# Kernel tuning notes

Hardware: AMD Instinct MI355X
Metric: run time of the kernel (lower is better)

## Reference

```python
import jax, jax.numpy as jnp
import numpy as np

USER = 50000
ITEM = 50000
N = USER + ITEM
LATDIM = 64
N_EDGES = 3200000
GNN_LAYERS = 2
RIS_ADJ_LAMBDA = 0.2
RIS_LAMBDA = 0.5
LEAK = 0.2


def l2norm(x, eps=1e-12):
    # F.normalize(x, dim=1)
    n = jnp.sqrt(jnp.sum(x * x, axis=1, keepdims=True))
    return x / jnp.maximum(n, eps)


def spmm(rows, cols, vals, x):
    # sparse [N,N] @ dense [N,D] via gather + segment-sum
    return jax.ops.segment_sum(vals[:, None] * x[cols], rows, num_segments=N)


def gcn_layer(rows, cols, vals, embeds, att_w):
    e = spmm(rows, cols, vals, embeds)                     # [N, D]
    scores = e @ att_w                                     # [N]
    att = jax.nn.softmax(scores, axis=0)[:, None]          # softmax over nodes
    return jax.nn.leaky_relu(e * att, negative_slope=LEAK) # dropout = identity (eval)


def setup_inputs() -> dict:
    key = jax.random.key(0)
    ks = jax.random.split(key, 16)
    d = {}
    for i, pre in enumerate(["adj", "img", "txt"]):
        d[pre + "_rows"] = jax.random.randint(ks[3 * i], (N_EDGES,), 0, N, dtype=jnp.int32)
        d[pre + "_cols"] = jax.random.randint(ks[3 * i + 1], (N_EDGES,), 0, N, dtype=jnp.int32)
        d[pre + "_vals"] = jax.random.uniform(ks[3 * i + 2], (N_EDGES,), dtype=jnp.float32)
    d["u_embeds"] = jax.random.normal(ks[9], (USER, LATDIM), dtype=jnp.float32) * 0.1
    d["i_embeds"] = jax.random.normal(ks[10], (ITEM, LATDIM), dtype=jnp.float32) * 0.1
    d["img_W"] = jax.random.normal(ks[11], (1024, LATDIM), dtype=jnp.float32) * 0.03
    d["img_b"] = jnp.zeros((LATDIM,), dtype=jnp.float32)
    d["txt_W"] = jax.random.normal(ks[12], (384, LATDIM), dtype=jnp.float32) * 0.05
    d["txt_b"] = jnp.zeros((LATDIM,), dtype=jnp.float32)
    d["modal_weight"] = jnp.array([0.5, 0.5], dtype=jnp.float32)
    d["att_w"] = jax.random.normal(ks[13], (GNN_LAYERS, LATDIM), dtype=jnp.float32) * 0.1
    d["image_embedding"] = jax.random.normal(ks[14], (USER, 1024), dtype=jnp.float32)
    d["text_embedding"] = jax.random.normal(ks[15], (USER, 384), dtype=jnp.float32)
    return d


def reference(adj_rows, adj_cols, adj_vals,
              img_rows, img_cols, img_vals,
              txt_rows, txt_cols, txt_vals,
              u_embeds, i_embeds,
              img_W, img_b, txt_W, txt_b,
              modal_weight, att_w,
              image_embedding, text_embedding):
    # modality projection (args.trans == 1: Linear layers)
    image_feats = image_embedding @ img_W + img_b          # [item, D]
    text_feats = text_embedding @ txt_W + txt_b            # [item, D]
    weight = jax.nn.softmax(modal_weight)

    e0 = jnp.concatenate([u_embeds, i_embeds])             # [N, D]

    embeds_image_adj = spmm(img_rows, img_cols, img_vals, e0)
    embeds_image = jnp.concatenate([u_embeds, l2norm(image_feats)])
    embeds_image_ = jnp.concatenate([embeds_image[:USER], i_embeds])
    embeds_image_ = spmm(adj_rows, adj_cols, adj_vals, embeds_image_)
    embeds_image = embeds_image + embeds_image_

    embeds_text_adj = spmm(txt_rows, txt_cols, txt_vals, e0)
    embeds_text = jnp.concatenate([u_embeds, l2norm(text_feats)])
    embeds_text = spmm(adj_rows, adj_cols, adj_vals, embeds_text)
    embeds_text_ = jnp.concatenate([embeds_text[:USER], i_embeds])
    embeds_text_ = spmm(adj_rows, adj_cols, adj_vals, embeds_text_)
    embeds_text = embeds_text + embeds_text_

    embeds_image = embeds_image + RIS_ADJ_LAMBDA * embeds_image_adj
    embeds_text = embeds_text + RIS_ADJ_LAMBDA * embeds_text_adj
    embeds_modal = weight[0] * embeds_image + weight[1] * embeds_text

    embeds = embeds_modal
    total = embeds_modal
    for l in range(GNN_LAYERS):
        embeds = gcn_layer(adj_rows, adj_cols, adj_vals, embeds, att_w[l])
        total = total + embeds
    out = total + RIS_LAMBDA * l2norm(embeds_modal)
    return out[:USER], out[USER:]
```

## Files before the change

kernel.cpp:

```cpp
#include <hip/hip_runtime.h>
#include <hip/hip_bf16.h>

#define LEAK 0.2f

__device__ __forceinline__ float wave_sum(float p) {
#pragma unroll
  for (int m = 1; m < 64; m <<= 1) p += __shfl_xor(p, m);
  return p;
}

__device__ __forceinline__ int wave_scan_incl(int v) {
  int lane = threadIdx.x & 63;
#pragma unroll
  for (int d = 1; d < 64; d <<= 1) {
    int t = __shfl_up(v, d);
    if (lane >= d) v += t;
  }
  return v;
}

__global__ __launch_bounds__(256) void gemm_bias(
    const float* __restrict__ A, const float* __restrict__ W,
    const float* __restrict__ bias, float* __restrict__ out, int M, int K)
{
  __shared__ float As[64 * 132];
  __shared__ float Wt[64 * 132];
  const int tid = threadIdx.x;
  const int lane = tid & 63, wave = tid >> 6;
  const int c0 = lane & 15;
  const int rsub = lane >> 4;
  const int rloc = wave * 16 + rsub * 4;
  const int rowBase = blockIdx.x * 64;

  float acc[4][4];
#pragma unroll
  for (int r = 0; r < 4; ++r)
#pragma unroll
    for (int i = 0; i < 4; ++i) acc[r][i] = 0.f;

  for (int kc = 0; kc < K; kc += 128) {
    __syncthreads();
#pragma unroll
    for (int j = 0; j < 8; ++j) {
      int idx = tid + j * 256;
      int row = idx >> 5, k4 = idx & 31;
      int gr = rowBase + row;
      int gk = kc + k4 * 4;
      float4 av = make_float4(0.f, 0.f, 0.f, 0.f);
      if (gr < M && gk < K) av = *(const float4*)(A + (size_t)gr * K + gk);
      *(float4*)(As + row * 132 + k4 * 4) = av;
    }
#pragma unroll
    for (int j = 0; j < 8; ++j) {
      int idx = tid + j * 256;
      int k = idx >> 4, c4 = (idx & 15) * 4;
      int gk = kc + k;
      float4 wv = make_float4(0.f, 0.f, 0.f, 0.f);
      if (gk < K) wv = *(const float4*)(W + (size_t)gk * 64 + c4);
      Wt[(c4 + 0) * 132 + k] = wv.x;
      Wt[(c4 + 1) * 132 + k] = wv.y;
      Wt[(c4 + 2) * 132 + k] = wv.z;
      Wt[(c4 + 3) * 132 + k] = wv.w;
    }
    __syncthreads();
#pragma unroll 4
    for (int kk = 0; kk < 128; kk += 4) {
      float4 a[4], w[4];
#pragma unroll
      for (int r = 0; r < 4; ++r) a[r] = *(const float4*)(As + (rloc + r) * 132 + kk);
#pragma unroll
      for (int i = 0; i < 4; ++i) w[i] = *(const float4*)(Wt + (c0 + 16 * i) * 132 + kk);
#pragma unroll
      for (int r = 0; r < 4; ++r)
#pragma unroll
        for (int i = 0; i < 4; ++i)
          acc[r][i] += a[r].x * w[i].x + a[r].y * w[i].y + a[r].z * w[i].z + a[r].w * w[i].w;
    }
  }
  float bv[4];
#pragma unroll
  for (int i = 0; i < 4; ++i) bv[i] = bias[c0 + 16 * i];
#pragma unroll
  for (int r = 0; r < 4; ++r) {
    int gr = rowBase + rloc + r;
    if (gr < M) {
#pragma unroll
      for (int i = 0; i < 4; ++i)
        out[(size_t)gr * 64 + c0 + 16 * i] = acc[r][i] + bv[i];
    }
  }
}

__global__ void l2norm_rows(float* __restrict__ x, int M)
{
  int lane = threadIdx.x & 63;
  int wid = (blockIdx.x * blockDim.x + threadIdx.x) >> 6;
  int nw = (gridDim.x * blockDim.x) >> 6;
  for (int n = wid; n < M; n += nw) {
    float v = x[(size_t)n * 64 + lane];
    float ss = wave_sum(v * v);
    float nrm = fmaxf(sqrtf(ss), 1e-12f);
    x[(size_t)n * 64 + lane] = v / nrm;
  }
}

__global__ void count_rows(const int* __restrict__ rows, int nedges, int* __restrict__ deg)
{
  int idx = blockIdx.x * blockDim.x + threadIdx.x;
  int stride = gridDim.x * blockDim.x;
  for (int e = idx; e < nedges; e += stride) atomicAdd(&deg[rows[e]], 1);
}

__global__ void block_reduce_deg(const int* __restrict__ deg, int n, int* __restrict__ bsum)
{
  __shared__ int wt[4];
  int idx = blockIdx.x * 256 + threadIdx.x;
  int v = (idx < n) ? deg[idx] : 0;
#pragma unroll
  for (int m = 1; m < 64; m <<= 1) v += __shfl_xor(v, m);
  if ((threadIdx.x & 63) == 0) wt[threadIdx.x >> 6] = v;
  __syncthreads();
  if (threadIdx.x == 0) bsum[blockIdx.x] = wt[0] + wt[1] + wt[2] + wt[3];
}

__global__ void scan_bsums(int* __restrict__ bsum, int nb)
{
  int lane = threadIdx.x;
  int carry = 0;
  for (int base = 0; base < nb; base += 64) {
    int idx = base + lane;
    int v = (idx < nb) ? bsum[idx] : 0;
    int sv = wave_scan_incl(v);
    if (idx < nb) bsum[idx] = sv - v + carry;
    carry += __shfl(sv, 63);
  }
}

__global__ void block_scan_write(const int* __restrict__ deg, const int* __restrict__ boff,
                                 int n, int* __restrict__ rowptr, int* __restrict__ cursor)
{
  __shared__ int wt[4];
  int idx = blockIdx.x * 256 + threadIdx.x;
  int v = (idx < n) ? deg[idx] : 0;
  int sv = wave_scan_incl(v);
  if ((threadIdx.x & 63) == 63) wt[threadIdx.x >> 6] = sv;
  __syncthreads();
  int w = threadIdx.x >> 6;
  int wo = 0;
#pragma unroll
  for (int k = 0; k < 4; ++k) if (k < w) wo += wt[k];
  int excl = sv - v + wo + boff[blockIdx.x];
  if (idx < n) { rowptr[idx] = excl; cursor[idx] = excl; }
  if (idx == n - 1) rowptr[n] = excl + v;
}

__global__ void scatter_edges(const int* __restrict__ rows, const int* __restrict__ cols,
                              const float* __restrict__ vals, int nedges,
                              int* __restrict__ cursor, int* __restrict__ ecol,
                              float* __restrict__ eval)
{
  int idx = blockIdx.x * blockDim.x + threadIdx.x;
  int stride = gridDim.x * blockDim.x;
  for (int e = idx; e < nedges; e += stride) {
    int r = rows[e];
    int pos = atomicAdd(&cursor[r], 1);
    ecol[pos] = cols[e];
    eval[pos] = vals[e];
  }
}

__global__ __launch_bounds__(256) void spmm_csr(
    const int* __restrict__ rowptr, const int* __restrict__ ecol,
    const float* __restrict__ eval,
    const float* __restrict__ lo, const float* __restrict__ hi, int user,
    float* __restrict__ out, float scale, int beta, int ntot,
    const float* __restrict__ attw, float* __restrict__ es, float* __restrict__ sumslot)
{
  const int lane = threadIdx.x & 63;
  int wid = (blockIdx.x * blockDim.x + threadIdx.x) >> 6;
  int nw = (gridDim.x * blockDim.x) >> 6;
  float aw = attw ? attw[lane] : 0.f;
  float sacc = 0.f;
  for (int r = wid; r < ntot; r += nw) {
    int s = rowptr[r], e_end = rowptr[r + 1];
    float acc = 0.f;
    for (int p = s; p < e_end; p += 64) {
      int e = p + lane;
      int c = 0; float v = 0.f;
      if (e < e_end) { c = ecol[e]; v = eval[e]; }
      int cnt = min(64, e_end - p);
      for (int i = 0; i < cnt; ++i) {
        int ci = __shfl(c, i);
        float vi = __shfl(v, i);
        const float* src = (ci < user) ? (lo + (size_t)ci * 64)
                                       : (hi + (size_t)(ci - user) * 64);
        acc = fmaf(vi, src[lane], acc);
      }
    }
    acc *= scale;
    if (beta) acc += out[(size_t)r * 64 + lane];
    out[(size_t)r * 64 + lane] = acc;
    if (attw) {
      float pdot = wave_sum(acc * aw);
      float ex = expf(pdot);
      if (lane == 0) es[r] = ex;
      sacc += ex;
    }
  }
  if (attw && lane == 0) atomicAdd(sumslot, sacc);
}

__global__ __launch_bounds__(256) void spmm_atomic(
    const int* __restrict__ rows, const int* __restrict__ cols,
    const float* __restrict__ vals,
    const float* __restrict__ lo, const float* __restrict__ hi, int user,
    float* __restrict__ out, float scale, int nedges)
{
  int lane = threadIdx.x & 63;
  int wid = (blockIdx.x * blockDim.x + threadIdx.x) >> 6;
  int nw = (gridDim.x * blockDim.x) >> 6;
  for (int base = wid * 64; base < nedges; base += nw * 64) {
    int e = base + lane;
    int c = 0, r = 0;
    float v = 0.f;
    if (e < nedges) { c = cols[e]; r = rows[e]; v = vals[e] * scale; }
    int cnt = min(64, nedges - base);
    for (int i = 0; i < cnt; ++i) {
      int ci = __shfl(c, i);
      int ri = __shfl(r, i);
      float vi = __shfl(v, i);
      const float* src = (ci < user) ? (lo + (size_t)ci * 64)
                                     : (hi + (size_t)(ci - user) * 64);
      atomicAdd(out + (size_t)ri * 64 + lane, vi * src[lane]);
    }
  }
}

__global__ void modal_kernel(const float* __restrict__ u, const float* __restrict__ imgn,
                             const float* __restrict__ acc, const float* __restrict__ stxt,
                             const float* __restrict__ t1, const float* __restrict__ t2,
                             const float* __restrict__ mw,
                             float* __restrict__ modal, float* __restrict__ total,
                             int user, int ntot)
{
  size_t idx = (size_t)blockIdx.x * blockDim.x + threadIdx.x;
  size_t tot = (size_t)ntot * 64;
  if (idx >= tot) return;
  int n = (int)(idx >> 6);
  float m0 = mw[0], m1 = mw[1];
  float mx = fmaxf(m0, m1);
  float e0 = expf(m0 - mx), e1 = expf(m1 - mx);
  float w0 = e0 / (e0 + e1), w1 = e1 / (e0 + e1);
  float bi = (n < user) ? u[idx] : imgn[idx - (size_t)user * 64];
  float ei = bi + acc[idx];
  float et = t1[idx] + t2[idx] + stxt[idx];
  float m = w0 * ei + w1 * et;
  modal[idx] = m;
  total[idx] = m;
}

__global__ void scores_kernel(const float* __restrict__ E, const float* __restrict__ attw,
                              float* __restrict__ es, float* __restrict__ sumslot, int ntot)
{
  int lane = threadIdx.x & 63;
  int wid = (blockIdx.x * blockDim.x + threadIdx.x) >> 6;
  int nw = (gridDim.x * blockDim.x) >> 6;
  float aw = attw[lane];
  float acc = 0.f;
  for (int n = wid; n < ntot; n += nw) {
    float p = E[(size_t)n * 64 + lane] * aw;
    p = wave_sum(p);
    float ex = expf(p);
    if (lane == 0) es[n] = ex;
    acc += ex;
  }
  if (lane == 0) atomicAdd(sumslot, acc);
}

__global__ void apply_att(const float* __restrict__ E, const float* __restrict__ es,
                          const float* __restrict__ sumslot,
                          float* __restrict__ cur, float* __restrict__ total, int ntot)
{
  size_t idx = (size_t)blockIdx.x * blockDim.x + threadIdx.x;
  size_t tot = (size_t)ntot * 64;
  if (idx >= tot) return;
  int n = (int)(idx >> 6);
  float att = es[n] / sumslot[0];
  float x = E[idx] * att;
  x = (x >= 0.f) ? x : LEAK * x;
  cur[idx] = x;
  total[idx] += x;
}

__global__ void final_norm_add(const float* __restrict__ modal, float* __restrict__ out, int ntot)
{
  int lane = threadIdx.x & 63;
  int wid = (blockIdx.x * blockDim.x + threadIdx.x) >> 6;
  int nw = (gridDim.x * blockDim.x) >> 6;
  for (int n = wid; n < ntot; n += nw) {
    float m = modal[(size_t)n * 64 + lane];
    float ss = wave_sum(m * m);
    float inv = 0.5f / fmaxf(sqrtf(ss), 1e-12f);
    out[(size_t)n * 64 + lane] += m * inv;
  }
}

extern "C" void kernel_launch(void* const* d_in, const int* in_sizes, int n_in,
                              void* d_out, int out_size, void* d_ws, size_t ws_size,
                              hipStream_t stream)
{
  const int*   adj_r = (const int*)d_in[0];
  const int*   adj_c = (const int*)d_in[1];
  const float* adj_v = (const float*)d_in[2];
  const int*   img_r = (const int*)d_in[3];
  const int*   img_c = (const int*)d_in[4];
  const float* img_v = (const float*)d_in[5];
  const int*   txt_r = (const int*)d_in[6];
  const int*   txt_c = (const int*)d_in[7];
  const float* txt_v = (const float*)d_in[8];
  const float* u_emb = (const float*)d_in[9];
  const float* i_emb = (const float*)d_in[10];
  const float* img_W = (const float*)d_in[11];
  const float* img_b = (const float*)d_in[12];
  const float* txt_W = (const float*)d_in[13];
  const float* txt_b = (const float*)d_in[14];
  const float* mw    = (const float*)d_in[15];
  const float* att_w = (const float*)d_in[16];
  const float* img_e = (const float*)d_in[17];
  const float* txt_e = (const float*)d_in[18];

  const int E1 = in_sizes[0], E2 = in_sizes[3], E3 = in_sizes[6];
  const int user = in_sizes[9] / 64;
  const int item = in_sizes[10] / 64;
  const int ntot = user + item;
  const int Kimg = in_sizes[11] / 64;
  const int Ktxt = in_sizes[13] / 64;
  const int Mimg = in_sizes[17] / Kimg;
  const int Mtxt = in_sizes[18] / Ktxt;

  char* basep = (char*)d_ws;
  size_t off = 0;
  auto alc = [&](size_t nb) -> char* {
    char* p = basep + off;
    off = (off + nb + 255) & ~(size_t)255;
    return p;
  };

  float* imgn  = (float*)alc((size_t)Mimg * 64 * 4);
  float* txtn  = (float*)alc((size_t)Mtxt * 64 * 4);
  float* accB  = (float*)alc((size_t)ntot * 64 * 4);
  float* stxt  = (float*)alc((size_t)ntot * 64 * 4);
  float* t1    = (float*)alc((size_t)ntot * 64 * 4);
  float* modal = (float*)alc((size_t)ntot * 64 * 4);
  float* es    = (float*)alc((size_t)ntot * 4);
  float* sums  = (float*)alc(256);
  int*   deg   = (int*)alc((size_t)ntot * 4);
  int*   bsum  = (int*)alc(4096);
  int*   rpA   = (int*)alc((size_t)(ntot + 1) * 4);
  int*   curA  = (int*)alc((size_t)ntot * 4);
  int*   ecolA = (int*)alc((size_t)E1 * 4);
  float* evalA = (float*)alc((size_t)E1 * 4);
  size_t adj_need = off;
  const int Emax = (E2 > E3) ? E2 : E3;
  int*   rpT   = (int*)alc((size_t)(ntot + 1) * 4);
  int*   curT  = (int*)alc((size_t)ntot * 4);
  int*   ecolT = (int*)alc((size_t)Emax * 4);
  float* evalT = (float*)alc((size_t)Emax * 4);
  size_t full_need = off;

  const bool useA = ws_size >= adj_need;
  const bool useT = ws_size >= full_need;

  float* t2    = (float*)d_out;
  float* total = (float*)d_out;
  float* E   = accB;
  float* cur = stxt;

  const size_t nbytes = (size_t)ntot * 64 * sizeof(float);
  hipMemsetAsync(sums, 0, 256, stream);

  gemm_bias<<<(Mimg + 63) / 64, 256, 0, stream>>>(img_e, img_W, img_b, imgn, Mimg, Kimg);
  gemm_bias<<<(Mtxt + 63) / 64, 256, 0, stream>>>(txt_e, txt_W, txt_b, txtn, Mtxt, Ktxt);
  l2norm_rows<<<256, 256, 0, stream>>>(imgn, Mimg);
  l2norm_rows<<<256, 256, 0, stream>>>(txtn, Mtxt);

  const int nb = (ntot + 255) / 256;
  auto build = [&](const int* rr, const int* cc, const float* vv, int ne,
                   int* rp, int* curp, int* ec, float* ev) {
    hipMemsetAsync(deg, 0, (size_t)ntot * 4, stream);
    count_rows<<<1024, 256, 0, stream>>>(rr, ne, deg);
    block_reduce_deg<<<nb, 256, 0, stream>>>(deg, ntot, bsum);
    scan_bsums<<<1, 64, 0, stream>>>(bsum, nb);
    block_scan_write<<<nb, 256, 0, stream>>>(deg, bsum, ntot, rp, curp);
    scatter_edges<<<1024, 256, 0, stream>>>(rr, cc, vv, ne, curp, ec, ev);
  };

  const int SG = 2048;
  const int SB = 4096;
  const int blk = (int)(((size_t)ntot * 64 + 255) / 256);

  if (useA) {
    build(adj_r, adj_c, adj_v, E1, rpA, curA, ecolA, evalA);
    spmm_csr<<<SG, 256, 0, stream>>>(rpA, ecolA, evalA, u_emb, i_emb, user,
                                     accB, 1.0f, 0, ntot, nullptr, nullptr, nullptr);
    if (useT) {
      build(img_r, img_c, img_v, E2, rpT, curT, ecolT, evalT);
      spmm_csr<<<SG, 256, 0, stream>>>(rpT, ecolT, evalT, u_emb, i_emb, user,
                                       accB, 0.2f, 1, ntot, nullptr, nullptr, nullptr);
    } else {
      spmm_atomic<<<SB, 256, 0, stream>>>(img_r, img_c, img_v, u_emb, i_emb, user,
                                          accB, 0.2f, E2);
    }
    if (useT) {
      build(txt_r, txt_c, txt_v, E3, rpT, curT, ecolT, evalT);
      spmm_csr<<<SG, 256, 0, stream>>>(rpT, ecolT, evalT, u_emb, i_emb, user,
                                       stxt, 0.2f, 0, ntot, nullptr, nullptr, nullptr);
    } else {
      hipMemsetAsync(stxt, 0, nbytes, stream);
      spmm_atomic<<<SB, 256, 0, stream>>>(txt_r, txt_c, txt_v, u_emb, i_emb, user,
                                          stxt, 0.2f, E3);
    }
    spmm_csr<<<SG, 256, 0, stream>>>(rpA, ecolA, evalA, u_emb, txtn, user,
                                     t1, 1.0f, 0, ntot, nullptr, nullptr, nullptr);
    spmm_csr<<<SG, 256, 0, stream>>>(rpA, ecolA, evalA, t1, i_emb, user,
                                     t2, 1.0f, 0, ntot, nullptr, nullptr, nullptr);
  } else {
    hipMemsetAsync(accB, 0, nbytes, stream);
    hipMemsetAsync(stxt, 0, nbytes, stream);
    hipMemsetAsync(t1,   0, nbytes, stream);
    hipMemsetAsync(t2,   0, nbytes, stream);
    spmm_atomic<<<SB, 256, 0, stream>>>(adj_r, adj_c, adj_v, u_emb, i_emb, user, accB, 1.0f, E1);
    spmm_atomic<<<SB, 256, 0, stream>>>(img_r, img_c, img_v, u_emb, i_emb, user, accB, 0.2f, E2);
    spmm_atomic<<<SB, 256, 0, stream>>>(txt_r, txt_c, txt_v, u_emb, i_emb, user, stxt, 0.2f, E3);
    spmm_atomic<<<SB, 256, 0, stream>>>(adj_r, adj_c, adj_v, u_emb, txtn, user, t1, 1.0f, E1);
    spmm_atomic<<<SB, 256, 0, stream>>>(adj_r, adj_c, adj_v, t1, i_emb, user, t2, 1.0f, E1);
  }

  modal_kernel<<<blk, 256, 0, stream>>>(u_emb, imgn, accB, stxt, t1, t2, mw,
                                        modal, total, user, ntot);

  for (int l = 0; l < 2; ++l) {
    const float* src = (l == 0) ? modal : cur;
    if (useA) {
      spmm_csr<<<SG, 256, 0, stream>>>(rpA, ecolA, evalA, src, src + (size_t)user * 64, user,
                                       E, 1.0f, 0, ntot, att_w + (size_t)l * 64, es, sums + l);
    } else {
      hipMemsetAsync(E, 0, nbytes, stream);
      spmm_atomic<<<SB, 256, 0, stream>>>(adj_r, adj_c, adj_v, src, src + (size_t)user * 64,
                                          user, E, 1.0f, E1);
      scores_kernel<<<256, 256, 0, stream>>>(E, att_w + (size_t)l * 64, es, sums + l, ntot);
    }
    apply_att<<<blk, 256, 0, stream>>>(E, es, sums + l, cur, total, ntot);
  }
  final_norm_add<<<256, 256, 0, stream>>>(modal, total, ntot);
}
```

Baseline: 3.415 ms.

## Pack CSR edges as int2, unroll SpMM gathers, fuse dual adjacency SpMMs

Stores CSR column and value together as one int2 per edge, so a single load fetches both and the shuffle-based broadcast is replaced by wave-uniform loads. Unrolls the SpMM row loop four-way with independent accumulators to keep more gathers in flight. Fuses the two adjacency SpMMs that share the same sparse matrix and user embeddings into one dual-output kernel, so the edge list is traversed once. Also raises grid sizes for the count, scatter and SpMM launches. The cost is a different floating-point summation order and higher register use.

```diff
diff --git a/kernel.cpp b/kernel.cpp
--- a/kernel.cpp
+++ b/kernel.cpp
@@ -154,24 +154,22 @@
   if (idx == n - 1) rowptr[n] = excl + v;
 }
 
-__global__ void scatter_edges(const int* __restrict__ rows, const int* __restrict__ cols,
-                              const float* __restrict__ vals, int nedges,
-                              int* __restrict__ cursor, int* __restrict__ ecol,
-                              float* __restrict__ eval)
+__global__ __launch_bounds__(256) void scatter_edges_pair(
+    const int* __restrict__ rows, const int* __restrict__ cols,
+    const float* __restrict__ vals, int nedges,
+    int* __restrict__ cursor, int2* __restrict__ epair)
 {
   int idx = blockIdx.x * blockDim.x + threadIdx.x;
   int stride = gridDim.x * blockDim.x;
   for (int e = idx; e < nedges; e += stride) {
     int r = rows[e];
     int pos = atomicAdd(&cursor[r], 1);
-    ecol[pos] = cols[e];
-    eval[pos] = vals[e];
+    epair[pos] = make_int2(cols[e], __float_as_int(vals[e]));
   }
 }
 
 __global__ __launch_bounds__(256) void spmm_csr(
-    const int* __restrict__ rowptr, const int* __restrict__ ecol,
-    const float* __restrict__ eval,
+    const int* __restrict__ rowptr, const int2* __restrict__ ep,
     const float* __restrict__ lo, const float* __restrict__ hi, int user,
     float* __restrict__ out, float scale, int beta, int ntot,
     const float* __restrict__ attw, float* __restrict__ es, float* __restrict__ sumslot)
@@ -181,23 +179,29 @@
   int nw = (gridDim.x * blockDim.x) >> 6;
   float aw = attw ? attw[lane] : 0.f;
   float sacc = 0.f;
-  for (int r = wid; r < ntot; r += nw) {
+  for (int r0 = wid; r0 < ntot; r0 += nw) {
+    const int r = __builtin_amdgcn_readfirstlane(r0);
     int s = rowptr[r], e_end = rowptr[r + 1];
-    float acc = 0.f;
-    for (int p = s; p < e_end; p += 64) {
-      int e = p + lane;
-      int c = 0; float v = 0.f;
-      if (e < e_end) { c = ecol[e]; v = eval[e]; }
-      int cnt = min(64, e_end - p);
-      for (int i = 0; i < cnt; ++i) {
-        int ci = __shfl(c, i);
-        float vi = __shfl(v, i);
-        const float* src = (ci < user) ? (lo + (size_t)ci * 64)
-                                       : (hi + (size_t)(ci - user) * 64);
-        acc = fmaf(vi, src[lane], acc);
-      }
-    }
-    acc *= scale;
+    float a0 = 0.f, a1 = 0.f, a2 = 0.f, a3 = 0.f;
+    int e = s;
+    for (; e + 4 <= e_end; e += 4) {
+      int2 p0 = ep[e], p1 = ep[e + 1], p2 = ep[e + 2], p3 = ep[e + 3];
+      const float* s0 = (p0.x < user) ? (lo + (size_t)p0.x * 64) : (hi + (size_t)(p0.x - user) * 64);
+      const float* s1 = (p1.x < user) ? (lo + (size_t)p1.x * 64) : (hi + (size_t)(p1.x - user) * 64);
+      const float* s2 = (p2.x < user) ? (lo + (size_t)p2.x * 64) : (hi + (size_t)(p2.x - user) * 64);
+      const float* s3 = (p3.x < user) ? (lo + (size_t)p3.x * 64) : (hi + (size_t)(p3.x - user) * 64);
+      float g0 = s0[lane], g1 = s1[lane], g2 = s2[lane], g3 = s3[lane];
+      a0 = fmaf(__int_as_float(p0.y), g0, a0);
+      a1 = fmaf(__int_as_float(p1.y), g1, a1);
+      a2 = fmaf(__int_as_float(p2.y), g2, a2);
+      a3 = fmaf(__int_as_float(p3.y), g3, a3);
+    }
+    for (; e < e_end; ++e) {
+      int2 p = ep[e];
+      const float* sp = (p.x < user) ? (lo + (size_t)p.x * 64) : (hi + (size_t)(p.x - user) * 64);
+      a0 = fmaf(__int_as_float(p.y), sp[lane], a0);
+    }
+    float acc = ((a0 + a1) + (a2 + a3)) * scale;
     if (beta) acc += out[(size_t)r * 64 + lane];
     out[(size_t)r * 64 + lane] = acc;
     if (attw) {
@@ -208,6 +212,46 @@
     }
   }
   if (attw && lane == 0) atomicAdd(sumslot, sacc);
+}
+
+__global__ __launch_bounds__(256) void spmm_csr_dual(
+    const int* __restrict__ rowptr, const int2* __restrict__ ep,
+    const float* __restrict__ lo, const float* __restrict__ hiA,
+    const float* __restrict__ hiB, int user,
+    float* __restrict__ outA, float* __restrict__ outB, int ntot)
+{
+  const int lane = threadIdx.x & 63;
+  int wid = (blockIdx.x * blockDim.x + threadIdx.x) >> 6;
+  int nw = (gridDim.x * blockDim.x) >> 6;
+  for (int r0 = wid; r0 < ntot; r0 += nw) {
+    const int r = __builtin_amdgcn_readfirstlane(r0);
+    int s = rowptr[r], e_end = rowptr[r + 1];
+    float a0 = 0.f, a1 = 0.f, b0 = 0.f, b1 = 0.f;
+    int e = s;
+    for (; e + 2 <= e_end; e += 2) {
+      int2 p0 = ep[e], p1 = ep[e + 1];
+      const float* sa0 = (p0.x < user) ? (lo + (size_t)p0.x * 64) : (hiA + (size_t)(p0.x - user) * 64);
+      const float* sb0 = (p0.x < user) ? (lo + (size_t)p0.x * 64) : (hiB + (size_t)(p0.x - user) * 64);
+      const float* sa1 = (p1.x < user) ? (lo + (size_t)p1.x * 64) : (hiA + (size_t)(p1.x - user) * 64);
+      const float* sb1 = (p1.x < user) ? (lo + (size_t)p1.x * 64) : (hiB + (size_t)(p1.x - user) * 64);
+      float ga0 = sa0[lane], gb0 = sb0[lane], ga1 = sa1[lane], gb1 = sb1[lane];
+      float v0 = __int_as_float(p0.y), v1 = __int_as_float(p1.y);
+      a0 = fmaf(v0, ga0, a0);
+      b0 = fmaf(v0, gb0, b0);
+      a1 = fmaf(v1, ga1, a1);
+      b1 = fmaf(v1, gb1, b1);
+    }
+    for (; e < e_end; ++e) {
+      int2 p = ep[e];
+      const float* sa = (p.x < user) ? (lo + (size_t)p.x * 64) : (hiA + (size_t)(p.x - user) * 64);
+      const float* sb = (p.x < user) ? (lo + (size_t)p.x * 64) : (hiB + (size_t)(p.x - user) * 64);
+      float v = __int_as_float(p.y);
+      a0 = fmaf(v, sa[lane], a0);
+      b0 = fmaf(v, sb[lane], b0);
+    }
+    outA[(size_t)r * 64 + lane] = a0 + a1;
+    outB[(size_t)r * 64 + lane] = b0 + b1;
+  }
 }
 
 __global__ __launch_bounds__(256) void spmm_atomic(
@@ -358,14 +402,12 @@
   int*   bsum  = (int*)alc(4096);
   int*   rpA   = (int*)alc((size_t)(ntot + 1) * 4);
   int*   curA  = (int*)alc((size_t)ntot * 4);
-  int*   ecolA = (int*)alc((size_t)E1 * 4);
-  float* evalA = (float*)alc((size_t)E1 * 4);
+  int2*  epA   = (int2*)alc((size_t)E1 * 8);
   size_t adj_need = off;
   const int Emax = (E2 > E3) ? E2 : E3;
   int*   rpT   = (int*)alc((size_t)(ntot + 1) * 4);
   int*   curT  = (int*)alc((size_t)ntot * 4);
-  int*   ecolT = (int*)alc((size_t)Emax * 4);
-  float* evalT = (float*)alc((size_t)Emax * 4);
+  int2*  epT   = (int2*)alc((size_t)Emax * 8);
   size_t full_need = off;
 
   const bool useA = ws_size >= adj_need;
@@ -386,43 +428,41 @@
 
   const int nb = (ntot + 255) / 256;
   auto build = [&](const int* rr, const int* cc, const float* vv, int ne,
-                   int* rp, int* curp, int* ec, float* ev) {
+                   int* rp, int* curp, int2* ep) {
     hipMemsetAsync(deg, 0, (size_t)ntot * 4, stream);
-    count_rows<<<1024, 256, 0, stream>>>(rr, ne, deg);
+    count_rows<<<2048, 256, 0, stream>>>(rr, ne, deg);
     block_reduce_deg<<<nb, 256, 0, stream>>>(deg, ntot, bsum);
     scan_bsums<<<1, 64, 0, stream>>>(bsum, nb);
     block_scan_write<<<nb, 256, 0, stream>>>(deg, bsum, ntot, rp, curp);
-    scatter_edges<<<1024, 256, 0, stream>>>(rr, cc, vv, ne, curp, ec, ev);
+    scatter_edges_pair<<<4096, 256, 0, stream>>>(rr, cc, vv, ne, curp, ep);
   };
 
-  const int SG = 2048;
+  const int SG = 4096;
   const int SB = 4096;
   const int blk = (int)(((size_t)ntot * 64 + 255) / 256);
 
   if (useA) {
-    build(adj_r, adj_c, adj_v, E1, rpA, curA, ecolA, evalA);
-    spmm_csr<<<SG, 256, 0, stream>>>(rpA, ecolA, evalA, u_emb, i_emb, user,
-                                     accB, 1.0f, 0, ntot, nullptr, nullptr, nullptr);
+    build(adj_r, adj_c, adj_v, E1, rpA, curA, epA);
+    spmm_csr_dual<<<SG, 256, 0, stream>>>(rpA, epA, u_emb, i_emb, txtn, user,
+                                          accB, t1, ntot);
     if (useT) {
-      build(img_r, img_c, img_v, E2, rpT, curT, ecolT, evalT);
-      spmm_csr<<<SG, 256, 0, stream>>>(rpT, ecolT, evalT, u_emb, i_emb, user,
+      build(img_r, img_c, img_v, E2, rpT, curT, epT);
+      spmm_csr<<<SG, 256, 0, stream>>>(rpT, epT, u_emb, i_emb, user,
                                        accB, 0.2f, 1, ntot, nullptr, nullptr, nullptr);
     } else {
       spmm_atomic<<<SB, 256, 0, stream>>>(img_r, img_c, img_v, u_emb, i_emb, user,
                                           accB, 0.2f, E2);
     }
     if (useT) {
-      build(txt_r, txt_c, txt_v, E3, rpT, curT, ecolT, evalT);
-      spmm_csr<<<SG, 256, 0, stream>>>(rpT, ecolT, evalT, u_emb, i_emb, user,
+      build(txt_r, txt_c, txt_v, E3, rpT, curT, epT);
+      spmm_csr<<<SG, 256, 0, stream>>>(rpT, epT, u_emb, i_emb, user,
                                        stxt, 0.2f, 0, ntot, nullptr, nullptr, nullptr);
     } else {
       hipMemsetAsync(stxt, 0, nbytes, stream);
       spmm_atomic<<<SB, 256, 0, stream>>>(txt_r, txt_c, txt_v, u_emb, i_emb, user,
                                           stxt, 0.2f, E3);
     }
-    spmm_csr<<<SG, 256, 0, stream>>>(rpA, ecolA, evalA, u_emb, txtn, user,
-                                     t1, 1.0f, 0, ntot, nullptr, nullptr, nullptr);
-    spmm_csr<<<SG, 256, 0, stream>>>(rpA, ecolA, evalA, t1, i_emb, user,
+    spmm_csr<<<SG, 256, 0, stream>>>(rpA, epA, t1, i_emb, user,
                                      t2, 1.0f, 0, ntot, nullptr, nullptr, nullptr);
   } else {
     hipMemsetAsync(accB, 0, nbytes, stream);
@@ -442,7 +482,7 @@
   for (int l = 0; l < 2; ++l) {
     const float* src = (l == 0) ? modal : cur;
     if (useA) {
-      spmm_csr<<<SG, 256, 0, stream>>>(rpA, ecolA, evalA, src, src + (size_t)user * 64, user,
+      spmm_csr<<<SG, 256, 0, stream>>>(rpA, epA, src, src + (size_t)user * 64, user,
                                        E, 1.0f, 0, ntot, att_w + (size_t)l * 64, es, sums + l);
     } else {
       hipMemsetAsync(E, 0, nbytes, stream);
```

New measurement: 2.971 ms. -13.0%, faster.
